# Performance work log

Hardware: AMD Instinct MI355X
Metric: run time of the kernel (lower is better)

## Reference

```python
import jax, jax.numpy as jnp
import numpy as np

N_TOK = 384
VOCAB = 50000
N_POS = 52
WDIM = 512
HDIM = 1024
FEAT_DIM = 3 * 16  # np.repeat([len,start,end],16)


def setup_inputs() -> dict:
    key = jax.random.key(0)
    ks = jax.random.split(key, 10)
    s = 0.02  # init scale
    return {
        "sentence": jax.random.randint(ks[0], (N_TOK,), 0, VOCAB),
        "pos_tags": jax.random.randint(ks[1], (N_TOK,), 0, N_POS),
        "We_wrd": jax.random.normal(ks[2], (VOCAB, WDIM), jnp.float32) * s,
        "We_pos": jax.random.normal(ks[3], (N_POS, WDIM), jnp.float32) * s,
        "W_dan1": jax.random.normal(ks[4], (2 * WDIM, HDIM), jnp.float32) * s,
        "b_dan1": jnp.zeros((HDIM,), jnp.float32),
        "W_dan2": jax.random.normal(ks[5], (HDIM, HDIM), jnp.float32) * s,
        "b_dan2": jnp.zeros((HDIM,), jnp.float32),
        "W_s1": jax.random.normal(ks[6], (HDIM + FEAT_DIM, HDIM), jnp.float32) * s,
        "b_s1": jnp.zeros((HDIM,), jnp.float32),
        "W_s2": jax.random.normal(ks[7], (HDIM, 1), jnp.float32) * s,
        "b_s2": jnp.zeros((1,), jnp.float32),
    }


def reference(sentence, pos_tags, We_wrd, We_pos, W_dan1, b_dan1, W_dan2, b_dan2, W_s1, b_s1, W_s2, b_s2):
    n = sentence.shape[0]
    # per-token embedding: concat(pos, word) as in score() with use_pos=True -> [n, 2*wdim]
    emb = jnp.concatenate([We_pos[pos_tags], We_wrd[sentence]], axis=-1)
    # prefix sums so every span mean is O(1): pref[k] = sum of emb[:k]
    pref = jnp.concatenate([jnp.zeros((1, emb.shape[1]), emb.dtype), jnp.cumsum(emb, axis=0)], axis=0)
    # all spans (i, j) with i <= j, as in the double loop over i..n-1, j..n-1
    i_idx, j_idx = np.triu_indices(n)  # static shapes, S = n(n+1)/2
    i_idx = jnp.asarray(i_idx)
    j_idx = jnp.asarray(j_idx)
    end = j_idx + 1
    length = (end - i_idx).astype(emb.dtype)
    # DAN encoder: mean of span embeddings -> 2 relu layers (config['layer']=2)
    mean = (pref[end] - pref[i_idx]) / length[:, None]            # [S, 2*wdim]
    h = jax.nn.relu(mean @ W_dan1 + b_dan1)                        # [S, hdim]
    h = jax.nn.relu(h @ W_dan2 + b_dan2)                           # [S, hdim]
    # phrase feats: np.repeat([len, start, end], 16) -> [S, 48]
    feats = jnp.repeat(jnp.stack([length, i_idx.astype(emb.dtype), end.astype(emb.dtype)], axis=1), 16, axis=1)
    rep = jnp.concatenate([h, feats], axis=1)                      # [S, hdim+48]
    # Wpscore MLP: Linear(ph_dim+48 -> hdim) + relu, Linear(hdim -> 1)
    h2 = jax.nn.relu(rep @ W_s1 + b_s1)
    scores = (h2 @ W_s2 + b_s2)[:, 0]                              # [S]
    return scores
```

## Files before the change

kernel.cpp:

```cpp
#include <hip/hip_runtime.h>

#define NTOK  384
#define SPANS 73920
#define MTILES 584
#define MPAD  (MTILES * 128)
#define HD    1024
#define BK    32
#define KTS   (HD / BK)
#define YSLICE ((size_t)NTOK * HD)

typedef unsigned short u16;
typedef __attribute__((ext_vector_type(8))) short short8;
typedef __attribute__((ext_vector_type(4))) float floatx4;

#define VMCNT_IMM(N) (((N) & 0xF) | (((N) >> 4) << 14) | (0x7 << 4) | (0xF << 8))

__device__ __forceinline__ u16 f2bu(float x) {
  union { float f; unsigned u; } un; un.f = x;
  unsigned r = un.u + 0x7fffu + ((un.u >> 16) & 1u);
  return (u16)(r >> 16);
}

__device__ __forceinline__ void gld_lds16(const void* g, void* l) {
  __builtin_amdgcn_global_load_lds(
      (const __attribute__((address_space(1))) void*)g,
      (__attribute__((address_space(3))) void*)l, 16, 0, 0);
}

__global__ void prep_misc(const int* __restrict__ sent, const int* __restrict__ pos,
                          const float* __restrict__ Wwrd, const float* __restrict__ Wpos,
                          u16* __restrict__ embB,
                          int* __restrict__ spI, int* __restrict__ spE, float* __restrict__ spInv,
                          float* __restrict__ scores, const float* __restrict__ bs2,
                          const float* __restrict__ Wd1, const float* __restrict__ Wd2,
                          const float* __restrict__ Ws1,
                          u16* __restrict__ o1, u16* __restrict__ o2, u16* __restrict__ o3,
                          float* __restrict__ S0, float* __restrict__ S1v, float* __restrict__ S2v) {
  __shared__ u16 tile[32][33];
  int bx = blockIdx.x;
  if (bx < 3072) {
    int w = bx >> 10, rem = bx & 1023;
    int tk = rem >> 5, tn = rem & 31;
    const float* src = (w == 0) ? Wd1 : ((w == 1) ? Wd2 : Ws1);
    u16* dst = (w == 0) ? o1 : ((w == 1) ? o2 : o3);
    int x = threadIdx.x & 31, y = threadIdx.x >> 5;
    int k0 = tk * 32, n0 = tn * 32;
    for (int yy = 0; yy < 32; yy += 8)
      tile[y + yy][x] = f2bu(src[(size_t)(k0 + y + yy) * HD + n0 + x]);
    __syncthreads();
    for (int yy = 0; yy < 32; yy += 8)
      dst[(size_t)(n0 + y + yy) * HD + k0 + x] = tile[x][y + yy];
  } else if (bx < 3072 + NTOK) {
    int t = bx - 3072;
    int c = threadIdx.x;
    int pt = pos[t], st = sent[t];
    #pragma unroll
    for (int u = 0; u < 4; ++u) {
      int col = u * 256 + c;
      float v = (col < 512) ? Wpos[(size_t)pt * 512 + col]
                            : Wwrd[(size_t)st * 512 + (col - 512)];
      embB[(size_t)t * HD + col] = f2bu(v);
    }
  } else if (bx < 3072 + NTOK + 292) {
    int rf = (bx - 3072 - NTOK) * 256 + threadIdx.x;
    if (rf >= MPAD) return;
    int s = rf < SPANS ? rf : SPANS - 1;
    const int n = NTOK;
    double tn2 = 2.0 * n + 1.0;
    int i = (int)((tn2 - sqrt(tn2 * tn2 - 8.0 * (double)s)) * 0.5);
    if (i < 0) i = 0;
    if (i > n - 1) i = n - 1;
    #define OFF(ii) (((ii) * (2 * n - (ii) + 1)) / 2)
    while (i + 1 <= n - 1 && OFF(i + 1) <= s) ++i;
    while (i > 0 && OFF(i) > s) --i;
    int j = i + (s - OFF(i));
    #undef OFF
    spI[rf] = i;
    spE[rf] = j + 1;
    spInv[rf] = 1.0f / (float)(j + 1 - i);
    if (rf < SPANS) scores[rf] = bs2[0];
  } else {
    int c = (bx - 3072 - NTOK - 292) * 256 + threadIdx.x;
    if (c >= HD) return;
    float a = 0.f, b = 0.f, d = 0.f;
    for (int r = 0; r < 16; ++r) {
      a += Ws1[(size_t)(1024 + r) * HD + c];
      b += Ws1[(size_t)(1040 + r) * HD + c];
      d += Ws1[(size_t)(1056 + r) * HD + c];
    }
    S0[c] = a; S1v[c] = b; S2v[c] = d;
  }
}

__global__ void yscan(const float* __restrict__ Y, float* __restrict__ Qp) {
  __shared__ float buf[NTOK];
  int c = blockIdx.x;
  int t = threadIdx.x;
  size_t idx = (size_t)t * HD + c;
  buf[t] = Y[idx] + Y[idx + YSLICE] + Y[idx + 2 * YSLICE] + Y[idx + 3 * YSLICE];
  __syncthreads();
  #pragma unroll
  for (int off = 1; off < NTOK; off <<= 1) {
    float add = (t >= off) ? buf[t - off] : 0.f;
    __syncthreads();
    buf[t] += add;
    __syncthreads();
  }
  if (t == 0) Qp[c] = 0.f;
  Qp[(size_t)(t + 1) * HD + c] = buf[t];
}

__global__ void expand(const float* __restrict__ Qp, const int* __restrict__ spI,
                       const int* __restrict__ spE, const float* __restrict__ spInv,
                       const float* __restrict__ b1, u16* __restrict__ out) {
  int gid = blockIdx.x * 256 + threadIdx.x;
  int row = gid >> 7;
  int c0 = (gid & 127) << 3;
  int i = spI[row], e = spE[row];
  float inv = spInv[row];
  const float* pe = Qp + (size_t)e * HD + c0;
  const float* pi = Qp + (size_t)i * HD + c0;
  const float* bb = b1 + c0;
  u16 tmp[8];
  #pragma unroll
  for (int u = 0; u < 8; ++u) {
    float v = (pe[u] - pi[u]) * inv + bb[u];
    v = v > 0.f ? v : 0.f;
    tmp[u] = f2bu(v);
  }
  *(uint4*)(out + (size_t)row * HD + c0) = *(const uint4*)tmp;
}

template <int EPI>
__global__ __launch_bounds__(256, 3) void gemm_bt(
    const u16* __restrict__ A, const u16* __restrict__ Bt,
    const float* __restrict__ bias, u16* __restrict__ C, float* __restrict__ Cf,
    const int* __restrict__ spI, const int* __restrict__ spE,
    const float* __restrict__ S0, const float* __restrict__ S1v, const float* __restrict__ S2v,
    const float* __restrict__ Ws2, float* __restrict__ scores) {
  __shared__ u16 As[2][128 * BK];
  __shared__ u16 Bs[2][128 * BK];
  int bx = blockIdx.x;
  int mt, nt, ks = 0, KT0 = 0, KT1 = KTS;
  if (EPI == 2) {
    int rem = bx & 31;
    nt = rem & 7; ks = rem >> 3; mt = bx >> 5;
    KT0 = ks * 8; KT1 = KT0 + 8;
  } else {
    int xcd = bx & 7, k = bx >> 3;
    nt = k & 7;
    mt = xcd + 8 * (k >> 3);
  }
  int m0 = mt * 128, n0 = nt * 128;
  int t = threadIdx.x, lane = t & 63, wid = t >> 6;
  int wm = wid >> 1, wn = wid & 1;
  int q = lane >> 4, r = lane & 15;

  floatx4 acc[4][4] = {};

  int dsub = (lane & 7) ^ ((lane >> 3) & 7);
  int row0 = wid * 16 + 2 * (lane >> 3) + (dsub >> 2);
  int voff = row0 * HD + (dsub & 3) * 8;
  const u16* gA0 = A  + (size_t)m0 * HD;
  const u16* gB0 = Bt + (size_t)n0 * HD;
  int ldsOff0 = wid * 512;
  int ldsOff1 = 2048 + wid * 512;

  auto stage = [&](int kt, int b) {
    const u16* pa = gA0 + voff + kt * BK;
    const u16* pb = gB0 + voff + kt * BK;
    gld_lds16(pa,                   &As[b][ldsOff0]);
    gld_lds16(pa + (size_t)64 * HD, &As[b][ldsOff1]);
    gld_lds16(pb,                   &Bs[b][ldsOff0]);
    gld_lds16(pb + (size_t)64 * HD, &Bs[b][ldsOff1]);
  };

  int oct = (((r & 1) << 2) + q) ^ ((r >> 1) & 7);
  int aoff[4], boff[4];
  #pragma unroll
  for (int x = 0; x < 4; ++x) {
    aoff[x] = (wm * 32 + x * 8 + (r >> 1)) * 64 + oct * 8;
    boff[x] = (wn * 32 + x * 8 + (r >> 1)) * 64 + oct * 8;
  }

  short8 af[4], bf[4];
  auto preload = [&](int b) {
    #pragma unroll
    for (int x = 0; x < 4; ++x) af[x] = *(const short8*)(&As[b][aoff[x]]);
    #pragma unroll
    for (int x = 0; x < 4; ++x) bf[x] = *(const short8*)(&Bs[b][boff[x]]);
  };
  auto mfma_burst = [&]() {
    #pragma unroll
    for (int ni = 0; ni < 4; ++ni)
      #pragma unroll
      for (int mi = 0; mi < 4; ++mi)
        acc[mi][ni] = __builtin_amdgcn_mfma_f32_16x16x32_bf16(af[mi], bf[ni], acc[mi][ni], 0, 0, 0);
  };

  stage(KT0, 0);
  stage(KT0 + 1, 1);
  __builtin_amdgcn_s_waitcnt(VMCNT_IMM(4));
  __builtin_amdgcn_s_barrier();
  preload(0);
  #pragma unroll 1
  for (int kt = KT0; kt < KT1; ++kt) {
    int cur = kt & 1;
    mfma_burst();
    __builtin_amdgcn_s_waitcnt(VMCNT_IMM(0));
    __builtin_amdgcn_s_barrier();
    if (kt + 2 < KT1) stage(kt + 2, cur);
    if (kt + 1 < KT1) preload(cur ^ 1);
  }

  if (EPI == 2) {
    float* Cfk = Cf + (size_t)ks * YSLICE;
    #pragma unroll
    for (int mi = 0; mi < 4; ++mi) {
      int rowb = m0 + wm * 64 + mi * 16 + q * 4;
      #pragma unroll
      for (int ni = 0; ni < 4; ++ni) {
        int col = n0 + wn * 64 + ni * 16 + r;
        #pragma unroll
        for (int e = 0; e < 4; ++e)
          Cfk[(size_t)(rowb + e) * HD + col] = acc[mi][ni][e];
      }
    }
  } else if (EPI == 0) {
    #pragma unroll
    for (int mi = 0; mi < 4; ++mi) {
      int rowb = m0 + wm * 64 + mi * 16 + q * 4;
      #pragma unroll
      for (int ni = 0; ni < 4; ++ni) {
        int col = n0 + wn * 64 + ni * 16 + r;
        float bcol = bias[col];
        #pragma unroll
        for (int e = 0; e < 4; ++e) {
          float v = acc[mi][ni][e] + bcol;
          v = v > 0.f ? v : 0.f;
          C[(size_t)(rowb + e) * HD + col] = f2bu(v);
        }
      }
    }
  } else {
    float bcol[4], s0c[4], s1c[4], s2c[4], wsc[4];
    #pragma unroll
    for (int ni = 0; ni < 4; ++ni) {
      int col = n0 + wn * 64 + ni * 16 + r;
      bcol[ni] = bias[col]; s0c[ni] = S0[col]; s1c[ni] = S1v[col];
      s2c[ni] = S2v[col];  wsc[ni] = Ws2[col];
    }
    #pragma unroll
    for (int mi = 0; mi < 4; ++mi) {
      int rowb = m0 + wm * 64 + mi * 16 + q * 4;
      #pragma unroll
      for (int e = 0; e < 4; ++e) {
        int row = rowb + e;
        float fi = (float)spI[row];
        float fe = (float)spE[row];
        float fl = fe - fi;
        float p = 0.f;
        #pragma unroll
        for (int ni = 0; ni < 4; ++ni) {
          float v = acc[mi][ni][e] + bcol[ni] + fl * s0c[ni] + fi * s1c[ni] + fe * s2c[ni];
          v = v > 0.f ? v : 0.f;
          p += v * wsc[ni];
        }
        p += __shfl_xor(p, 1);
        p += __shfl_xor(p, 2);
        p += __shfl_xor(p, 4);
        p += __shfl_xor(p, 8);
        if (r == 0 && row < SPANS) atomicAdd(&scores[row], p);
      }
    }
  }
}

extern "C" void kernel_launch(void* const* d_in, const int* in_sizes, int n_in,
                              void* d_out, int out_size, void* d_ws, size_t ws_size,
                              hipStream_t stream) {
  const int*   sent = (const int*)d_in[0];
  const int*   pos  = (const int*)d_in[1];
  const float* Wwrd = (const float*)d_in[2];
  const float* Wpos = (const float*)d_in[3];
  const float* Wd1  = (const float*)d_in[4];
  const float* bd1  = (const float*)d_in[5];
  const float* Wd2  = (const float*)d_in[6];
  const float* bd2  = (const float*)d_in[7];
  const float* Ws1  = (const float*)d_in[8];
  const float* bs1  = (const float*)d_in[9];
  const float* Ws2  = (const float*)d_in[10];
  const float* bs2  = (const float*)d_in[11];
  float* scores = (float*)d_out;

  char* w = (char*)d_ws;
  size_t o = 0;
  auto alloc = [&](size_t bytes) {
    char* p = w + o;
    o = (o + bytes + 255) & ~(size_t)255;
    return p;
  };
  int*   spI   = (int*)  alloc((size_t)MPAD * 4);
  int*   spE   = (int*)  alloc((size_t)MPAD * 4);
  float* spInv = (float*)alloc((size_t)MPAD * 4);
  float* S0    = (float*)alloc(4096);
  float* S1v   = (float*)alloc(4096);
  float* S2v   = (float*)alloc(4096);
  u16*   embB  = (u16*)  alloc((size_t)NTOK * HD * 2);
  float* Ybuf  = (float*)alloc(4 * YSLICE * 4);
  float* Qp    = (float*)alloc((size_t)(NTOK + 1) * HD * 4);
  u16* Wd1t = (u16*)alloc((size_t)HD * HD * 2);
  u16* Wd2t = (u16*)alloc((size_t)HD * HD * 2);
  u16* Ws1t = (u16*)alloc((size_t)HD * HD * 2);
  u16* bufA = (u16*)alloc((size_t)MPAD * HD * 2);
  u16* bufB = (u16*)alloc((size_t)MPAD * HD * 2);

  prep_misc<<<3072 + NTOK + 292 + 4, 256, 0, stream>>>(
      sent, pos, Wwrd, Wpos, embB,
      spI, spE, spInv, scores, bs2,
      Wd1, Wd2, Ws1, Wd1t, Wd2t, Ws1t,
      S0, S1v, S2v);

  gemm_bt<2><<<96, 256, 0, stream>>>(embB, Wd1t, nullptr, nullptr, Ybuf,
                                     nullptr, nullptr, nullptr, nullptr, nullptr,
                                     nullptr, nullptr);
  yscan<<<HD, NTOK, 0, stream>>>(Ybuf, Qp);
  expand<<<MPAD / 2, 256, 0, stream>>>(Qp, spI, spE, spInv, bd1, bufA);

  gemm_bt<0><<<MTILES * 8, 256, 0, stream>>>(bufA, Wd2t, bd2, bufB, nullptr,
                                             nullptr, nullptr, nullptr, nullptr, nullptr,
                                             nullptr, nullptr);
  gemm_bt<1><<<MTILES * 8, 256, 0, stream>>>(bufB, Ws1t, bs1, nullptr, nullptr,
                                             spI, spE, S0, S1v, S2v, Ws2, scores);
}
```

Before: 579.2 us.

## Use 256x128 tiles with 512-thread blocks for the two big span GEMMs

Splits the old templated GEMM into a dedicated split-K kernel for the embedding projection and a new 512-thread kernel for the two large span GEMMs. The new kernel uses 256-row by 128-column tiles with eight waves, so each B tile staged into LDS is reused across twice as many A rows, and the grid is remapped so consecutive blocks spread across XCDs. This is meant to cut global and LDS traffic for the B operand and to lower block count. In exchange it uses more LDS per block, which may reduce occupancy.

```diff
diff --git a/kernel.cpp b/kernel.cpp
--- a/kernel.cpp
+++ b/kernel.cpp
@@ -2,8 +2,9 @@
 
 #define NTOK  384
 #define SPANS 73920
-#define MTILES 584
-#define MPAD  (MTILES * 128)
+#define MPAD  74752
+#define MT2   292
+#define GRID2 (MT2 * 8)
 #define HD    1024
 #define BK    32
 #define KTS   (HD / BK)
@@ -131,26 +132,14 @@
   *(uint4*)(out + (size_t)row * HD + c0) = *(const uint4*)tmp;
 }
 
-template <int EPI>
-__global__ __launch_bounds__(256, 3) void gemm_bt(
-    const u16* __restrict__ A, const u16* __restrict__ Bt,
-    const float* __restrict__ bias, u16* __restrict__ C, float* __restrict__ Cf,
-    const int* __restrict__ spI, const int* __restrict__ spE,
-    const float* __restrict__ S0, const float* __restrict__ S1v, const float* __restrict__ S2v,
-    const float* __restrict__ Ws2, float* __restrict__ scores) {
+__global__ __launch_bounds__(256, 3) void gemm_y(
+    const u16* __restrict__ A, const u16* __restrict__ Bt, float* __restrict__ Cf) {
   __shared__ u16 As[2][128 * BK];
   __shared__ u16 Bs[2][128 * BK];
   int bx = blockIdx.x;
-  int mt, nt, ks = 0, KT0 = 0, KT1 = KTS;
-  if (EPI == 2) {
-    int rem = bx & 31;
-    nt = rem & 7; ks = rem >> 3; mt = bx >> 5;
-    KT0 = ks * 8; KT1 = KT0 + 8;
-  } else {
-    int xcd = bx & 7, k = bx >> 3;
-    nt = k & 7;
-    mt = xcd + 8 * (k >> 3);
-  }
+  int rem = bx & 31;
+  int nt = rem & 7, ks = rem >> 3, mt = bx >> 5;
+  int KT0 = ks * 8, KT1 = KT0 + 8;
   int m0 = mt * 128, n0 = nt * 128;
   int t = threadIdx.x, lane = t & 63, wid = t >> 6;
   int wm = wid >> 1, wn = wid & 1;
@@ -189,13 +178,6 @@
     for (int x = 0; x < 4; ++x) af[x] = *(const short8*)(&As[b][aoff[x]]);
     #pragma unroll
     for (int x = 0; x < 4; ++x) bf[x] = *(const short8*)(&Bs[b][boff[x]]);
-  };
-  auto mfma_burst = [&]() {
-    #pragma unroll
-    for (int ni = 0; ni < 4; ++ni)
-      #pragma unroll
-      for (int mi = 0; mi < 4; ++mi)
-        acc[mi][ni] = __builtin_amdgcn_mfma_f32_16x16x32_bf16(af[mi], bf[ni], acc[mi][ni], 0, 0, 0);
   };
 
   stage(KT0, 0);
@@ -206,27 +188,103 @@
   #pragma unroll 1
   for (int kt = KT0; kt < KT1; ++kt) {
     int cur = kt & 1;
-    mfma_burst();
+    #pragma unroll
+    for (int ni = 0; ni < 4; ++ni)
+      #pragma unroll
+      for (int mi = 0; mi < 4; ++mi)
+        acc[mi][ni] = __builtin_amdgcn_mfma_f32_16x16x32_bf16(af[mi], bf[ni], acc[mi][ni], 0, 0, 0);
     __builtin_amdgcn_s_waitcnt(VMCNT_IMM(0));
     __builtin_amdgcn_s_barrier();
     if (kt + 2 < KT1) stage(kt + 2, cur);
     if (kt + 1 < KT1) preload(cur ^ 1);
   }
 
-  if (EPI == 2) {
-    float* Cfk = Cf + (size_t)ks * YSLICE;
-    #pragma unroll
-    for (int mi = 0; mi < 4; ++mi) {
-      int rowb = m0 + wm * 64 + mi * 16 + q * 4;
-      #pragma unroll
-      for (int ni = 0; ni < 4; ++ni) {
-        int col = n0 + wn * 64 + ni * 16 + r;
-        #pragma unroll
-        for (int e = 0; e < 4; ++e)
-          Cfk[(size_t)(rowb + e) * HD + col] = acc[mi][ni][e];
-      }
-    }
-  } else if (EPI == 0) {
+  float* Cfk = Cf + (size_t)ks * YSLICE;
+  #pragma unroll
+  for (int mi = 0; mi < 4; ++mi) {
+    int rowb = m0 + wm * 64 + mi * 16 + q * 4;
+    #pragma unroll
+    for (int ni = 0; ni < 4; ++ni) {
+      int col = n0 + wn * 64 + ni * 16 + r;
+      #pragma unroll
+      for (int e = 0; e < 4; ++e)
+        Cfk[(size_t)(rowb + e) * HD + col] = acc[mi][ni][e];
+    }
+  }
+}
+
+template <int EPI>
+__global__ __launch_bounds__(512, 4) void gemm2_bt(
+    const u16* __restrict__ A, const u16* __restrict__ Bt,
+    const float* __restrict__ bias, u16* __restrict__ C,
+    const int* __restrict__ spI, const int* __restrict__ spE,
+    const float* __restrict__ S0, const float* __restrict__ S1v, const float* __restrict__ S2v,
+    const float* __restrict__ Ws2, float* __restrict__ scores) {
+  __shared__ u16 As[2][8192];
+  __shared__ u16 Bs[2][4096];
+
+  int swz = (blockIdx.x & 7) * MT2 + (blockIdx.x >> 3);
+  int mt = swz >> 3, nt = swz & 7;
+  int m0 = mt * 256, n0 = nt * 128;
+  int t = threadIdx.x, lane = t & 63, wid = t >> 6;
+  int wm = wid >> 1, wn = wid & 1;
+  int q = lane >> 4, r = lane & 15;
+
+  floatx4 acc[4][4] = {};
+
+  int dsub = (lane & 7) ^ ((lane >> 3) & 7);
+  int row0 = wid * 16 + 2 * (lane >> 3) + (dsub >> 2);
+  int voff = row0 * HD + (dsub & 3) * 8;
+  const u16* gA0 = A  + (size_t)m0 * HD;
+  const u16* gB0 = Bt + (size_t)n0 * HD;
+  int ldsA0 = wid * 512;
+  int ldsA1 = 4096 + wid * 512;
+  int ldsB0 = wid * 512;
+
+  auto stage = [&](int kt, int b) {
+    const u16* pa = gA0 + voff + kt * BK;
+    const u16* pb = gB0 + voff + kt * BK;
+    gld_lds16(pa,                    &As[b][ldsA0]);
+    gld_lds16(pa + (size_t)128 * HD, &As[b][ldsA1]);
+    gld_lds16(pb,                    &Bs[b][ldsB0]);
+  };
+
+  int oct = (((r & 1) << 2) + q) ^ ((r >> 1) & 7);
+  int aoff[4], boff[4];
+  #pragma unroll
+  for (int x = 0; x < 4; ++x) {
+    aoff[x] = (wm * 32 + x * 8 + (r >> 1)) * 64 + oct * 8;
+    boff[x] = (wn * 32 + x * 8 + (r >> 1)) * 64 + oct * 8;
+  }
+
+  short8 af[4], bf[4];
+  auto preload = [&](int b) {
+    #pragma unroll
+    for (int x = 0; x < 4; ++x) af[x] = *(const short8*)(&As[b][aoff[x]]);
+    #pragma unroll
+    for (int x = 0; x < 4; ++x) bf[x] = *(const short8*)(&Bs[b][boff[x]]);
+  };
+
+  stage(0, 0);
+  stage(1, 1);
+  __builtin_amdgcn_s_waitcnt(VMCNT_IMM(3));
+  __builtin_amdgcn_s_barrier();
+  preload(0);
+  #pragma unroll 1
+  for (int kt = 0; kt < KTS; ++kt) {
+    int cur = kt & 1;
+    #pragma unroll
+    for (int ni = 0; ni < 4; ++ni)
+      #pragma unroll
+      for (int mi = 0; mi < 4; ++mi)
+        acc[mi][ni] = __builtin_amdgcn_mfma_f32_16x16x32_bf16(af[mi], bf[ni], acc[mi][ni], 0, 0, 0);
+    __builtin_amdgcn_s_waitcnt(VMCNT_IMM(0));
+    __builtin_amdgcn_s_barrier();
+    if (kt + 2 < KTS) stage(kt + 2, cur);
+    if (kt + 1 < KTS) preload(cur ^ 1);
+  }
+
+  if (EPI == 0) {
     #pragma unroll
     for (int mi = 0; mi < 4; ++mi) {
       int rowb = m0 + wm * 64 + mi * 16 + q * 4;
@@ -321,15 +379,13 @@
       Wd1, Wd2, Ws1, Wd1t, Wd2t, Ws1t,
       S0, S1v, S2v);
 
-  gemm_bt<2><<<96, 256, 0, stream>>>(embB, Wd1t, nullptr, nullptr, Ybuf,
-                                     nullptr, nullptr, nullptr, nullptr, nullptr,
-                                     nullptr, nullptr);
+  gemm_y<<<96, 256, 0, stream>>>(embB, Wd1t, Ybuf);
   yscan<<<HD, NTOK, 0, stream>>>(Ybuf, Qp);
   expand<<<MPAD / 2, 256, 0, stream>>>(Qp, spI, spE, spInv, bd1, bufA);
 
-  gemm_bt<0><<<MTILES * 8, 256, 0, stream>>>(bufA, Wd2t, bd2, bufB, nullptr,
-                                             nullptr, nullptr, nullptr, nullptr, nullptr,
-                                             nullptr, nullptr);
-  gemm_bt<1><<<MTILES * 8, 256, 0, stream>>>(bufB, Ws1t, bs1, nullptr, nullptr,
-                                             spI, spE, S0, S1v, S2v, Ws2, scores);
-}
+  gemm2_bt<0><<<GRID2, 512, 0, stream>>>(bufA, Wd2t, bd2, bufB,
+                                         nullptr, nullptr, nullptr, nullptr, nullptr,
+                                         nullptr, nullptr);
+  gemm2_bt<1><<<GRID2, 512, 0, stream>>>(bufB, Ws1t, bs1, nullptr,
+                                         spI, spE, S0, S1v, S2v, Ws2, scores);
+}
```

New measurement: 587.0 us. Within noise of the previous version (+1.4%).

## Prepack weights into MFMA fragment order and load B directly to registers

Applied to the files above, without the earlier changes.

Adds a kernel that rearranges each transposed weight matrix into MFMA fragment order. The GEMM then reads B fragments straight from global memory into registers instead of staging them through LDS. This halves the LDS footprint, so launch bounds rise to 4 blocks per CU, and the main loop is unrolled by two with ping-pong register buffers for B. The cost is one extra repack kernel, more registers for the double-buffered B fragments, and B loads that may be less coalesced or less reused across waves, since each wave now fetches its own B directly.

```diff
diff --git a/kernel.cpp b/kernel.cpp
--- a/kernel.cpp
+++ b/kernel.cpp
@@ -92,6 +92,23 @@
   }
 }
 
+__global__ void bfrag(const u16* __restrict__ t1, const u16* __restrict__ t2, const u16* __restrict__ t3,
+                      u16* __restrict__ f1, u16* __restrict__ f2, u16* __restrict__ f3) {
+  int b = blockIdx.x;
+  int w = b >> 10, rem = b & 1023;
+  int nt = rem >> 5, kt = rem & 31;
+  const u16* src = (w == 0) ? t1 : ((w == 1) ? t2 : t3);
+  u16* dst = (w == 0) ? f1 : ((w == 1) ? f2 : f3);
+  int t = threadIdx.x;
+  int ni = t >> 6, lane = t & 63, q = lane >> 4, r = lane & 15;
+  #pragma unroll
+  for (int wn = 0; wn < 2; ++wn) {
+    const u16* s = src + (size_t)(nt * 128 + wn * 64 + ni * 16 + r) * HD + kt * 32 + q * 8;
+    u16* d = dst + (size_t)nt * 131072 + kt * 4096 + wn * 2048 + ni * 512 + lane * 8;
+    *(short8*)d = *(const short8*)s;
+  }
+}
+
 __global__ void yscan(const float* __restrict__ Y, float* __restrict__ Qp) {
   __shared__ float buf[NTOK];
   int c = blockIdx.x;
@@ -132,14 +149,13 @@
 }
 
 template <int EPI>
-__global__ __launch_bounds__(256, 3) void gemm_bt(
-    const u16* __restrict__ A, const u16* __restrict__ Bt,
+__global__ __launch_bounds__(256, 4) void gemm_bt(
+    const u16* __restrict__ A, const u16* __restrict__ Bf,
     const float* __restrict__ bias, u16* __restrict__ C, float* __restrict__ Cf,
     const int* __restrict__ spI, const int* __restrict__ spE,
     const float* __restrict__ S0, const float* __restrict__ S1v, const float* __restrict__ S2v,
     const float* __restrict__ Ws2, float* __restrict__ scores) {
   __shared__ u16 As[2][128 * BK];
-  __shared__ u16 Bs[2][128 * BK];
   int bx = blockIdx.x;
   int mt, nt, ks = 0, KT0 = 0, KT1 = KTS;
   if (EPI == 2) {
@@ -151,7 +167,8 @@
     nt = k & 7;
     mt = xcd + 8 * (k >> 3);
   }
-  int m0 = mt * 128, n0 = nt * 128;
+  int m0 = mt * 128;
+  int n0 = nt * 128;
   int t = threadIdx.x, lane = t & 63, wid = t >> 6;
   int wm = wid >> 1, wn = wid & 1;
   int q = lane >> 4, r = lane & 15;
@@ -161,36 +178,35 @@
   int dsub = (lane & 7) ^ ((lane >> 3) & 7);
   int row0 = wid * 16 + 2 * (lane >> 3) + (dsub >> 2);
   int voff = row0 * HD + (dsub & 3) * 8;
-  const u16* gA0 = A  + (size_t)m0 * HD;
-  const u16* gB0 = Bt + (size_t)n0 * HD;
+  const u16* gA0 = A + (size_t)m0 * HD;
   int ldsOff0 = wid * 512;
   int ldsOff1 = 2048 + wid * 512;
 
-  auto stage = [&](int kt, int b) {
+  auto stageA = [&](int kt, int b) {
     const u16* pa = gA0 + voff + kt * BK;
-    const u16* pb = gB0 + voff + kt * BK;
     gld_lds16(pa,                   &As[b][ldsOff0]);
     gld_lds16(pa + (size_t)64 * HD, &As[b][ldsOff1]);
-    gld_lds16(pb,                   &Bs[b][ldsOff0]);
-    gld_lds16(pb + (size_t)64 * HD, &Bs[b][ldsOff1]);
+  };
+
+  const u16* gBb = Bf + (size_t)nt * 131072 + wn * 2048 + lane * 8;
+  auto loadB = [&](int kt, short8 (&bf)[4]) {
+    #pragma unroll
+    for (int ni = 0; ni < 4; ++ni)
+      bf[ni] = *(const short8*)(gBb + (size_t)kt * 4096 + ni * 512);
   };
 
   int oct = (((r & 1) << 2) + q) ^ ((r >> 1) & 7);
-  int aoff[4], boff[4];
+  int aoff[4];
   #pragma unroll
-  for (int x = 0; x < 4; ++x) {
+  for (int x = 0; x < 4; ++x)
     aoff[x] = (wm * 32 + x * 8 + (r >> 1)) * 64 + oct * 8;
-    boff[x] = (wn * 32 + x * 8 + (r >> 1)) * 64 + oct * 8;
-  }
-
-  short8 af[4], bf[4];
-  auto preload = [&](int b) {
+
+  short8 af[4], bfA[4], bfB[4];
+  auto preloadA = [&](int b) {
     #pragma unroll
     for (int x = 0; x < 4; ++x) af[x] = *(const short8*)(&As[b][aoff[x]]);
-    #pragma unroll
-    for (int x = 0; x < 4; ++x) bf[x] = *(const short8*)(&Bs[b][boff[x]]);
-  };
-  auto mfma_burst = [&]() {
+  };
+  auto burst = [&](short8 (&bf)[4]) {
     #pragma unroll
     for (int ni = 0; ni < 4; ++ni)
       #pragma unroll
@@ -198,19 +214,26 @@
         acc[mi][ni] = __builtin_amdgcn_mfma_f32_16x16x32_bf16(af[mi], bf[ni], acc[mi][ni], 0, 0, 0);
   };
 
-  stage(KT0, 0);
-  stage(KT0 + 1, 1);
-  __builtin_amdgcn_s_waitcnt(VMCNT_IMM(4));
+  stageA(KT0, 0);
+  stageA(KT0 + 1, 1);
+  loadB(KT0, bfA);
+  loadB(KT0 + 1, bfB);
+  __builtin_amdgcn_s_waitcnt(VMCNT_IMM(0));
   __builtin_amdgcn_s_barrier();
-  preload(0);
+  preloadA(0);
+
   #pragma unroll 1
-  for (int kt = KT0; kt < KT1; ++kt) {
-    int cur = kt & 1;
-    mfma_burst();
+  for (int kt = KT0; kt < KT1; kt += 2) {
+    burst(bfA);
     __builtin_amdgcn_s_waitcnt(VMCNT_IMM(0));
     __builtin_amdgcn_s_barrier();
-    if (kt + 2 < KT1) stage(kt + 2, cur);
-    if (kt + 1 < KT1) preload(cur ^ 1);
+    if (kt + 2 < KT1) { stageA(kt + 2, 0); loadB(kt + 2, bfA); }
+    preloadA(1);
+    burst(bfB);
+    __builtin_amdgcn_s_waitcnt(VMCNT_IMM(0));
+    __builtin_amdgcn_s_barrier();
+    if (kt + 3 < KT1) { stageA(kt + 3, 1); loadB(kt + 3, bfB); }
+    if (kt + 2 < KT1) preloadA(0);
   }
 
   if (EPI == 2) {
@@ -312,6 +335,9 @@
   u16* Wd1t = (u16*)alloc((size_t)HD * HD * 2);
   u16* Wd2t = (u16*)alloc((size_t)HD * HD * 2);
   u16* Ws1t = (u16*)alloc((size_t)HD * HD * 2);
+  u16* Wd1f = (u16*)alloc((size_t)HD * HD * 2);
+  u16* Wd2f = (u16*)alloc((size_t)HD * HD * 2);
+  u16* Ws1f = (u16*)alloc((size_t)HD * HD * 2);
   u16* bufA = (u16*)alloc((size_t)MPAD * HD * 2);
   u16* bufB = (u16*)alloc((size_t)MPAD * HD * 2);
 
@@ -320,16 +346,17 @@
       spI, spE, spInv, scores, bs2,
       Wd1, Wd2, Ws1, Wd1t, Wd2t, Ws1t,
       S0, S1v, S2v);
-
-  gemm_bt<2><<<96, 256, 0, stream>>>(embB, Wd1t, nullptr, nullptr, Ybuf,
+  bfrag<<<3072, 256, 0, stream>>>(Wd1t, Wd2t, Ws1t, Wd1f, Wd2f, Ws1f);
+
+  gemm_bt<2><<<96, 256, 0, stream>>>(embB, Wd1f, nullptr, nullptr, Ybuf,
                                      nullptr, nullptr, nullptr, nullptr, nullptr,
                                      nullptr, nullptr);
   yscan<<<HD, NTOK, 0, stream>>>(Ybuf, Qp);
   expand<<<MPAD / 2, 256, 0, stream>>>(Qp, spI, spE, spInv, bd1, bufA);
 
-  gemm_bt<0><<<MTILES * 8, 256, 0, stream>>>(bufA, Wd2t, bd2, bufB, nullptr,
+  gemm_bt<0><<<MTILES * 8, 256, 0, stream>>>(bufA, Wd2f, bd2, bufB, nullptr,
                                              nullptr, nullptr, nullptr, nullptr, nullptr,
                                              nullptr, nullptr);
-  gemm_bt<1><<<MTILES * 8, 256, 0, stream>>>(bufB, Ws1t, bs1, nullptr, nullptr,
+  gemm_bt<1><<<MTILES * 8, 256, 0, stream>>>(bufB, Ws1f, bs1, nullptr, nullptr,
                                              spI, spE, S0, S1v, S2v, Ws2, scores);
 }
```

New measurement: 575.5 us. About the same (-0.6%).
